# Optimization experiments

Measured on AMD Instinct MI355X. Metric: run time of the kernel, lower is better.

## Reference

```python
import jax, jax.numpy as jnp
import numpy as np

D = 1024       # embedding_dim
H = 4096       # mlp_dim
E = 64         # num_experts
K = 3          # top-k
B, S = 2, 2048
C = 512


def setup_inputs() -> dict:
    key = jax.random.key(0)
    ks = jax.random.split(key, 6)
    s = 0.02
    return {
        "x": jax.random.normal(ks[0], (B, S, D), jnp.float32),
        "gate_w": jax.random.normal(ks[1], (D, E), jnp.float32) * s,
        "gate_b": jnp.zeros((E,), jnp.float32),
        "w1": jax.random.normal(ks[2], (E, D, H), jnp.float32) * s,
        "b1": jnp.zeros((E, H), jnp.float32),
        "w2": jax.random.normal(ks[3], (E, H, D), jnp.float32) * s,
        "b2": jnp.zeros((E, D), jnp.float32),
    }


def reference(x, gate_w, gate_b, w1, b1, w2, b2):
    xf = x.reshape(-1, D)                       # [T, D] flattened tokens
    T = xf.shape[0]
    # --- top-k gating (eval mode: clean logits, no noise) ---
    logits = xf @ gate_w + gate_b               # [T, E]
    top_l, top_i = jax.lax.top_k(logits, K)     # [T, K]
    gates = jax.nn.softmax(top_l, axis=-1)      # softmax over the k selected logits
    # --- token permutation / dispatch (capacity-based, order-preserving) ---
    fe = top_i.reshape(-1)                      # [T*K] expert id per assignment
    fg = gates.reshape(-1)                      # [T*K] gate per assignment
    tok = jnp.repeat(jnp.arange(T), K)          # [T*K] source token id
    oh = jax.nn.one_hot(fe, E, dtype=jnp.int32) # [T*K, E]
    pos = (jnp.cumsum(oh, axis=0) * oh).sum(-1) - 1  # slot within expert buffer
    valid = pos < C                             # capacity mask (C sized so nothing drops in practice)
    # scatter tokens into per-expert buffers; OOB (pos>=C) rows dropped
    buf = jnp.zeros((E, C, D), x.dtype).at[fe, pos].set(xf[tok], mode='drop')
    # --- grouped expert MLP: Linear -> exact GELU -> Linear ---
    h = jax.nn.gelu(jnp.einsum('ecd,edh->ech', buf, w1) + b1[:, None, :], approximate=False)
    y = jnp.einsum('ech,ehd->ecd', h, w2) + b2[:, None, :]  # [E, C, D]
    # --- gather back, gate, scatter-add combine ---
    rows = y[fe, jnp.minimum(pos, C - 1)] * (fg * valid.astype(x.dtype))[:, None]
    out = jnp.zeros_like(xf).at[tok].add(rows)
    return out.reshape(x.shape)
```

## Files before the change

kernel.cpp:

```cpp
#include <hip/hip_runtime.h>

#define TTOK 4096
#define DDIM 1024
#define HDIM 4096
#define NEXP 64
#define CAP  512
#define NASN (TTOK*3)

typedef unsigned short u16;
typedef __attribute__((ext_vector_type(8))) short s16x8;
typedef __attribute__((ext_vector_type(4))) short s16x4;
typedef __attribute__((ext_vector_type(4))) float f32x4;

__device__ __forceinline__ u16 f2bf(float f) {
  union { float f; unsigned u; } v; v.f = f;
  unsigned u = v.u;
  return (u16)((u + 0x7fffu + ((u >> 16) & 1u)) >> 16);
}

__device__ __forceinline__ void gl_lds16(const void* g, void* l) {
  __builtin_amdgcn_global_load_lds(
      (const __attribute__((address_space(1))) void*)g,
      (__attribute__((address_space(3))) void*)l, 16, 0, 0);
}

__global__ __launch_bounds__(256) void zero_out(float4* __restrict__ p, int n4) {
  int i = blockIdx.x * 256 + threadIdx.x;
  int st = gridDim.x * 256;
  for (; i < n4; i += st) p[i] = (float4){0.f, 0.f, 0.f, 0.f};
}

__global__ __launch_bounds__(512) void gate_topk(
    const float* __restrict__ x, const float* __restrict__ gw,
    const float* __restrict__ gb, int* __restrict__ fe, float* __restrict__ fg)
{
  int lane = threadIdx.x & 63;
  int wid  = threadIdx.x >> 6;
  int t = blockIdx.x * 8 + wid;
  const float* xr = x + (size_t)t * DDIM;
  float acc = gb[lane];
  #pragma unroll 4
  for (int d = 0; d < DDIM; d++) acc += xr[d] * gw[d * NEXP + lane];

  float v = acc;
  float bv[3]; int bi[3];
  #pragma unroll
  for (int j = 0; j < 3; j++) {
    float mv = v; int mi = lane;
    #pragma unroll
    for (int off = 32; off; off >>= 1) {
      float ov = __shfl_xor(mv, off);
      int   oi = __shfl_xor(mi, off);
      if (ov > mv || (ov == mv && oi < mi)) { mv = ov; mi = oi; }
    }
    bv[j] = mv; bi[j] = mi;
    if (lane == mi) v = -3.4e38f;
  }
  if (lane == 0) {
    float e1 = expf(bv[1] - bv[0]), e2 = expf(bv[2] - bv[0]);
    float inv = 1.0f / (1.0f + e1 + e2);
    fe[t*3+0] = bi[0]; fe[t*3+1] = bi[1]; fe[t*3+2] = bi[2];
    fg[t*3+0] = inv;   fg[t*3+1] = e1*inv; fg[t*3+2] = e2*inv;
  }
}

__global__ __launch_bounds__(64) void scan_pos(
    const int* __restrict__ fe, int* __restrict__ posA,
    int* __restrict__ s2a, int* __restrict__ cnt)
{
  int e = blockIdx.x, lane = threadIdx.x;
  int base = 0;
  for (int i0 = 0; i0 < NASN; i0 += 64) {
    int i = i0 + lane;
    bool m = (fe[i] == e);
    unsigned long long bal = __ballot(m);
    int below = __popcll(bal & ((1ull << lane) - 1ull));
    if (m) {
      int p = base + below;
      posA[i] = p;
      if (p < CAP) s2a[e * CAP + p] = i;
    }
    base += __popcll(bal);
  }
  if (lane == 0) cnt[e] = base < CAP ? base : CAP;
}

__global__ __launch_bounds__(64) void dispatch(
    const float* __restrict__ x, const int* __restrict__ fe,
    const int* __restrict__ posA, u16* __restrict__ bufA)
{
  int a = blockIdx.x;
  int p = posA[a];
  if (p >= CAP) return;
  int e = fe[a];
  int tok = a / 3;
  int l = threadIdx.x;
  const float4* xr = (const float4*)(x + (size_t)tok * DDIM);
  u16* dst = bufA + ((size_t)e * CAP + p) * DDIM;
  #pragma unroll
  for (int j = 0; j < 4; j++) {
    float4 v = xr[j * 64 + l];
    uint2 u;
    u.x = (unsigned)f2bf(v.x) | ((unsigned)f2bf(v.y) << 16);
    u.y = (unsigned)f2bf(v.z) | ((unsigned)f2bf(v.w) << 16);
    *(uint2*)(dst + (size_t)(j * 64 + l) * 4) = u;
  }
}

template<int KTOT, int NTOT, int EPI>
__global__ __launch_bounds__(256, 2) void moe_gemm(
    const u16* __restrict__ Abuf, const float* __restrict__ W,
    const float* __restrict__ bias, u16* __restrict__ hout,
    float* __restrict__ out, const int* __restrict__ cnt,
    const int* __restrict__ s2a, const float* __restrict__ fg, int g0)
{
  constexpr int NCT = NTOT / 128;
  constexpr int NT  = KTOT / 64;
  int NB = gridDim.x;
  int b = blockIdx.x;
  int L = (b & 7) * (NB >> 3) + (b >> 3);
  int tcol = L % NCT;
  int rt   = (L / NCT) & 1;
  int el   = L / (NCT * 2);
  int e    = g0 + el;
  int cnte = cnt[e];
  int c0   = rt * 256;
  if (c0 >= cnte) return;
  int n0 = tcol * 128;

  int tid = threadIdx.x, l = tid & 63, w = tid >> 6;

  __shared__ char AsB[256 * 128];
  __shared__ char BsB[128 * 136];

  const u16* Arows = Abuf + ((size_t)((EPI == 1 ? e : el)) * CAP + c0) * (size_t)KTOT;
  const float* We = W + (size_t)e * KTOT * NTOT;

  int bn4 = tid & 31, bkb = (tid >> 5) * 8;
  const float* Wt = We + (size_t)bkb * NTOT + n0 + bn4 * 4;
  char* BsW = BsB + (bn4 * 4) * 136 + bkb * 2;

  float4 brB4[8];
  #define LOADB(t) { \
    const float* p_ = Wt + (size_t)(t) * 64 * NTOT; \
    _Pragma("unroll") \
    for (int j_ = 0; j_ < 8; j_++) \
      brB4[j_] = *(const float4*)(p_ + (size_t)j_ * NTOT); \
    }
  #define STOREB() { \
    _Pragma("unroll") \
    for (int c_ = 0; c_ < 4; c_++) { \
      float v0_ = (c_==0?brB4[0].x:c_==1?brB4[0].y:c_==2?brB4[0].z:brB4[0].w); \
      float v1_ = (c_==0?brB4[1].x:c_==1?brB4[1].y:c_==2?brB4[1].z:brB4[1].w); \
      float v2_ = (c_==0?brB4[2].x:c_==1?brB4[2].y:c_==2?brB4[2].z:brB4[2].w); \
      float v3_ = (c_==0?brB4[3].x:c_==1?brB4[3].y:c_==2?brB4[3].z:brB4[3].w); \
      float v4_ = (c_==0?brB4[4].x:c_==1?brB4[4].y:c_==2?brB4[4].z:brB4[4].w); \
      float v5_ = (c_==0?brB4[5].x:c_==1?brB4[5].y:c_==2?brB4[5].z:brB4[5].w); \
      float v6_ = (c_==0?brB4[6].x:c_==1?brB4[6].y:c_==2?brB4[6].z:brB4[6].w); \
      float v7_ = (c_==0?brB4[7].x:c_==1?brB4[7].y:c_==2?brB4[7].z:brB4[7].w); \
      uint2 ua_, ub_; \
      ua_.x = (unsigned)f2bf(v0_) | ((unsigned)f2bf(v1_) << 16); \
      ua_.y = (unsigned)f2bf(v2_) | ((unsigned)f2bf(v3_) << 16); \
      ub_.x = (unsigned)f2bf(v4_) | ((unsigned)f2bf(v5_) << 16); \
      ub_.y = (unsigned)f2bf(v6_) | ((unsigned)f2bf(v7_) << 16); \
      *(uint2*)(BsW + c_ * 136) = ua_; \
      *(uint2*)(BsW + c_ * 136 + 8) = ub_; \
    } }

  f32x4 acc[4][8];
  #pragma unroll
  for (int m = 0; m < 4; m++)
    #pragma unroll
    for (int nn = 0; nn < 8; nn++)
      acc[m][nn] = (f32x4){0.f, 0.f, 0.f, 0.f};

  LOADB(0);

  for (int t = 0; t < NT; ++t) {
    #pragma unroll
    for (int i = 0; i < 8; i++) {
      int r = i * 32 + w * 8 + (l >> 3);
      int cswz = (l & 7) ^ (r & 7);
      const char* gsrc = (const char*)(Arows + (size_t)r * KTOT + (size_t)t * 64) + cswz * 16;
      gl_lds16(gsrc, AsB + (i * 32 + w * 8) * 128);
    }
    STOREB();
    __builtin_amdgcn_sched_barrier(0);
    if (t + 1 < NT) {
      LOADB(t + 1);
      __builtin_amdgcn_sched_barrier(0);
      asm volatile("s_waitcnt vmcnt(8)" ::: "memory");
    } else {
      asm volatile("s_waitcnt vmcnt(0)" ::: "memory");
    }
    asm volatile("s_waitcnt lgkmcnt(0)" ::: "memory");
    __builtin_amdgcn_sched_barrier(0);
    __builtin_amdgcn_s_barrier();
    __builtin_amdgcn_sched_barrier(0);

    #pragma unroll
    for (int k2 = 0; k2 < 2; k2++) {
      int kb = k2 * 32;
      s16x8 af[4], bf8[8];
      #pragma unroll
      for (int m = 0; m < 4; m++) {
        int R = w * 64 + m * 16 + (l & 15);
        int chunk = (kb >> 3) + (l >> 4);
        int sc = chunk ^ (R & 7);
        af[m] = *(const s16x8*)(AsB + R * 128 + sc * 16);
      }
      #pragma unroll
      for (int nn = 0; nn < 8; nn++) {
        int Nn = nn * 16 + (l & 15);
        int kk = kb + (l >> 4) * 8;
        const char* bp = BsB + Nn * 136 + kk * 2;
        union { s16x8 v8; s16x4 v4[2]; } bu;
        bu.v4[0] = *(const s16x4*)bp;
        bu.v4[1] = *(const s16x4*)(bp + 8);
        bf8[nn] = bu.v8;
      }
      #pragma unroll
      for (int m = 0; m < 4; m++)
        #pragma unroll
        for (int nn = 0; nn < 8; nn++)
          acc[m][nn] = __builtin_amdgcn_mfma_f32_16x16x32_bf16(af[m], bf8[nn], acc[m][nn], 0, 0, 0);
    }
    __builtin_amdgcn_s_barrier();
    __builtin_amdgcn_sched_barrier(0);
  }

  int lr = l >> 4, lc = l & 15;
  float bv[8];
  #pragma unroll
  for (int nn = 0; nn < 8; nn++) bv[nn] = bias[(size_t)e * NTOT + n0 + nn * 16 + lc];

  if (EPI == 1) {
    #pragma unroll
    for (int m = 0; m < 4; m++)
      #pragma unroll
      for (int q = 0; q < 4; q++) {
        int rowL = w * 64 + m * 16 + lr * 4 + q;
        if (c0 + rowL < cnte) {
          #pragma unroll
          for (int nn = 0; nn < 8; nn++) {
            float vv = acc[m][nn][q] + bv[nn];
            vv = 0.5f * vv * (1.0f + erff(vv * 0.70710678118f));
            hout[(size_t)(el * CAP + c0 + rowL) * NTOT + (n0 + nn * 16 + lc)] = f2bf(vv);
          }
        }
      }
  } else {
    #pragma unroll
    for (int m = 0; m < 4; m++) {
      int rowbase = w * 64 + m * 16 + lr * 4;
      #pragma unroll
      for (int q = 0; q < 4; q++) {
        int slot = c0 + rowbase + q;
        if (slot < cnte) {
          int aidx = s2a[e * CAP + slot];
          int tok = aidx / 3;
          float gg = fg[aidx];
          #pragma unroll
          for (int nn = 0; nn < 8; nn++) {
            float vv = (acc[m][nn][q] + bv[nn]) * gg;
            atomicAdd(out + (size_t)tok * DDIM + (n0 + nn * 16 + lc), vv);
          }
        }
      }
    }
  }
}

extern "C" void kernel_launch(void* const* d_in, const int* in_sizes, int n_in,
                              void* d_out, int out_size, void* d_ws, size_t ws_size,
                              hipStream_t stream) {
  (void)in_sizes; (void)n_in; (void)ws_size;
  const float* x  = (const float*)d_in[0];
  const float* gw = (const float*)d_in[1];
  const float* gb = (const float*)d_in[2];
  const float* w1 = (const float*)d_in[3];
  const float* b1 = (const float*)d_in[4];
  const float* w2 = (const float*)d_in[5];
  const float* b2 = (const float*)d_in[6];
  float* out = (float*)d_out;

  char* ws = (char*)d_ws;
  int*   fe   = (int*)(ws);
  float* fg   = (float*)(ws + 49152);
  int*   posA = (int*)(ws + 98304);
  int*   s2a  = (int*)(ws + 147456);
  int*   cnt  = (int*)(ws + 278528);
  u16*   bufA = (u16*)(ws + (1 << 20));
  u16*   hbuf = (u16*)(ws + (1 << 20) + 67108864ull);

  zero_out<<<1024, 256, 0, stream>>>((float4*)out, out_size / 4);
  gate_topk<<<TTOK / 8, 512, 0, stream>>>(x, gw, gb, fe, fg);
  scan_pos<<<NEXP, 64, 0, stream>>>(fe, posA, s2a, cnt);
  dispatch<<<NASN, 64, 0, stream>>>(x, fe, posA, bufA);

  moe_gemm<DDIM, HDIM, 1><<<NEXP * 2 * (HDIM / 128), 256, 0, stream>>>(
      bufA, w1, b1, hbuf, nullptr, cnt, nullptr, nullptr, 0);
  moe_gemm<HDIM, DDIM, 2><<<NEXP * 2 * (DDIM / 128), 256, 0, stream>>>(
      hbuf, w2, b2, nullptr, out, cnt, s2a, fg, 0);
}
```

Baseline: 694.4 us.

## Prefetch next A tile during MFMA and swizzle B LDS layout

Each wave now loads only the 64 A rows it consumes. It pulls its A fragments into registers for both k-halves, then issues the global-to-LDS loads for the next A tile before running the MFMAs. This overlaps A-tile latency with compute instead of serializing it at the top of each iteration. The padded 136-byte B stride is replaced by an unpadded 128-byte row with an XOR swizzle, which cuts LDS footprint and aims to avoid bank conflicts. In exchange, more A fragment registers stay live and there are extra lgkmcnt waits.

```diff
diff --git a/kernel.cpp b/kernel.cpp
--- a/kernel.cpp
+++ b/kernel.cpp
@@ -22,6 +22,10 @@
   __builtin_amdgcn_global_load_lds(
       (const __attribute__((address_space(1))) void*)g,
       (__attribute__((address_space(3))) void*)l, 16, 0, 0);
+}
+
+__device__ __forceinline__ int bswz(int row) {
+  return (((row >> 2) ^ ((row & 3) << 2)) & 15) << 3;
 }
 
 __global__ __launch_bounds__(256) void zero_out(float4* __restrict__ p, int n4) {
@@ -131,14 +135,13 @@
   int tid = threadIdx.x, l = tid & 63, w = tid >> 6;
 
   __shared__ char AsB[256 * 128];
-  __shared__ char BsB[128 * 136];
+  __shared__ char BsB[128 * 128];
 
   const u16* Arows = Abuf + ((size_t)((EPI == 1 ? e : el)) * CAP + c0) * (size_t)KTOT;
   const float* We = W + (size_t)e * KTOT * NTOT;
 
   int bn4 = tid & 31, bkb = (tid >> 5) * 8;
   const float* Wt = We + (size_t)bkb * NTOT + n0 + bn4 * 4;
-  char* BsW = BsB + (bn4 * 4) * 136 + bkb * 2;
 
   float4 brB4[8];
   #define LOADB(t) { \
@@ -163,9 +166,24 @@
       ua_.y = (unsigned)f2bf(v2_) | ((unsigned)f2bf(v3_) << 16); \
       ub_.x = (unsigned)f2bf(v4_) | ((unsigned)f2bf(v5_) << 16); \
       ub_.y = (unsigned)f2bf(v6_) | ((unsigned)f2bf(v7_) << 16); \
-      *(uint2*)(BsW + c_ * 136) = ua_; \
-      *(uint2*)(BsW + c_ * 136 + 8) = ub_; \
+      int row_ = bn4 * 4 + c_; \
+      int sw_  = bswz(row_); \
+      char* rb_ = BsB + row_ * 128; \
+      *(uint2*)(rb_ + ((bkb * 2) ^ sw_))     = ua_; \
+      *(uint2*)(rb_ + ((bkb * 2 + 8) ^ sw_)) = ub_; \
     } }
+
+  #define GLDS_A(t) { \
+    _Pragma("unroll") \
+    for (int i_ = 0; i_ < 8; i_++) { \
+      int rb_ = w * 64 + i_ * 8; \
+      int r_  = rb_ + (l >> 3); \
+      int cswz_ = (l & 7) ^ (r_ & 7); \
+      const char* gsrc_ = (const char*)(Arows + (size_t)r_ * KTOT + (size_t)(t) * 64) + cswz_ * 16; \
+      gl_lds16(gsrc_, AsB + rb_ * 128); \
+    } }
+
+  #define SB() __builtin_amdgcn_sched_barrier(0)
 
   f32x4 acc[4][8];
   #pragma unroll
@@ -174,59 +192,66 @@
     for (int nn = 0; nn < 8; nn++)
       acc[m][nn] = (f32x4){0.f, 0.f, 0.f, 0.f};
 
+  GLDS_A(0);
   LOADB(0);
 
   for (int t = 0; t < NT; ++t) {
-    #pragma unroll
-    for (int i = 0; i < 8; i++) {
-      int r = i * 32 + w * 8 + (l >> 3);
-      int cswz = (l & 7) ^ (r & 7);
-      const char* gsrc = (const char*)(Arows + (size_t)r * KTOT + (size_t)t * 64) + cswz * 16;
-      gl_lds16(gsrc, AsB + (i * 32 + w * 8) * 128);
-    }
     STOREB();
-    __builtin_amdgcn_sched_barrier(0);
+    SB();
     if (t + 1 < NT) {
       LOADB(t + 1);
-      __builtin_amdgcn_sched_barrier(0);
+      SB();
       asm volatile("s_waitcnt vmcnt(8)" ::: "memory");
     } else {
       asm volatile("s_waitcnt vmcnt(0)" ::: "memory");
     }
     asm volatile("s_waitcnt lgkmcnt(0)" ::: "memory");
-    __builtin_amdgcn_sched_barrier(0);
+    SB();
     __builtin_amdgcn_s_barrier();
-    __builtin_amdgcn_sched_barrier(0);
-
-    #pragma unroll
-    for (int k2 = 0; k2 < 2; k2++) {
-      int kb = k2 * 32;
-      s16x8 af[4], bf8[8];
+    SB();
+
+    {
+      s16x8 af[4][2];
       #pragma unroll
-      for (int m = 0; m < 4; m++) {
-        int R = w * 64 + m * 16 + (l & 15);
-        int chunk = (kb >> 3) + (l >> 4);
-        int sc = chunk ^ (R & 7);
-        af[m] = *(const s16x8*)(AsB + R * 128 + sc * 16);
+      for (int k2 = 0; k2 < 2; k2++) {
+        #pragma unroll
+        for (int m = 0; m < 4; m++) {
+          int R = w * 64 + m * 16 + (l & 15);
+          int chunk = k2 * 4 + (l >> 4);
+          int sc = chunk ^ (R & 7);
+          af[m][k2] = *(const s16x8*)(AsB + R * 128 + sc * 16);
+        }
       }
+      asm volatile("s_waitcnt lgkmcnt(0)" ::: "memory");
+      SB();
+      if (t + 1 < NT) { GLDS_A(t + 1); }
+      SB();
       #pragma unroll
-      for (int nn = 0; nn < 8; nn++) {
-        int Nn = nn * 16 + (l & 15);
-        int kk = kb + (l >> 4) * 8;
-        const char* bp = BsB + Nn * 136 + kk * 2;
-        union { s16x8 v8; s16x4 v4[2]; } bu;
-        bu.v4[0] = *(const s16x4*)bp;
-        bu.v4[1] = *(const s16x4*)(bp + 8);
-        bf8[nn] = bu.v8;
+      for (int k2 = 0; k2 < 2; k2++) {
+        int kb = k2 * 32;
+        s16x8 bf8[8];
+        #pragma unroll
+        for (int nn = 0; nn < 8; nn++) {
+          int Nn = nn * 16 + (l & 15);
+          int kk = kb + (l >> 4) * 8;
+          int o1 = (kk * 2) ^ bswz(Nn);
+          const char* bp = BsB + Nn * 128;
+          union { s16x8 v8; s16x4 v4[2]; } bu;
+          bu.v4[0] = *(const s16x4*)(bp + o1);
+          bu.v4[1] = *(const s16x4*)(bp + (o1 ^ 8));
+          bf8[nn] = bu.v8;
+        }
+        #pragma unroll
+        for (int m = 0; m < 4; m++)
+          #pragma unroll
+          for (int nn = 0; nn < 8; nn++)
+            acc[m][nn] = __builtin_amdgcn_mfma_f32_16x16x32_bf16(af[m][k2], bf8[nn], acc[m][nn], 0, 0, 0);
       }
-      #pragma unroll
-      for (int m = 0; m < 4; m++)
-        #pragma unroll
-        for (int nn = 0; nn < 8; nn++)
-          acc[m][nn] = __builtin_amdgcn_mfma_f32_16x16x32_bf16(af[m], bf8[nn], acc[m][nn], 0, 0, 0);
-    }
+    }
+    asm volatile("s_waitcnt lgkmcnt(0)" ::: "memory");
+    SB();
     __builtin_amdgcn_s_barrier();
-    __builtin_amdgcn_sched_barrier(0);
+    SB();
   }
 
   int lr = l >> 4, lc = l & 15;
```

Measured after the change: 1.072 ms. +54.4%, slower.

## Replace atomic scatter-add combine with per-expert store plus gather combine kernel

Applied to the files above, without the earlier changes.

The second expert GEMM now writes plain fp32 rows into a per-expert output buffer instead of atomically adding gated rows into the output. A new combine kernel gathers each token's three expert rows, applies the gate weights and writes the output directly, so the zero-fill kernel is no longer needed. This trades global atomic contention for an extra fp32 write and read of the expert output buffer plus one more kernel launch.

```diff
diff --git a/kernel.cpp b/kernel.cpp
--- a/kernel.cpp
+++ b/kernel.cpp
@@ -22,12 +22,6 @@
   __builtin_amdgcn_global_load_lds(
       (const __attribute__((address_space(1))) void*)g,
       (__attribute__((address_space(3))) void*)l, 16, 0, 0);
-}
-
-__global__ __launch_bounds__(256) void zero_out(float4* __restrict__ p, int n4) {
-  int i = blockIdx.x * 256 + threadIdx.x;
-  int st = gridDim.x * 256;
-  for (; i < n4; i += st) p[i] = (float4){0.f, 0.f, 0.f, 0.f};
 }
 
 __global__ __launch_bounds__(512) void gate_topk(
@@ -107,12 +101,32 @@
   }
 }
 
+__global__ __launch_bounds__(256) void combine(
+    const float* __restrict__ y, const int* __restrict__ fe,
+    const float* __restrict__ fg, const int* __restrict__ posA,
+    float* __restrict__ out)
+{
+  int t = blockIdx.x;
+  int d4 = threadIdx.x;
+  float4 s = (float4){0.f, 0.f, 0.f, 0.f};
+  #pragma unroll
+  for (int k = 0; k < 3; k++) {
+    int a = t * 3 + k;
+    int p = posA[a];
+    if (p < CAP) {
+      float g = fg[a];
+      float4 v = *(const float4*)(y + ((size_t)fe[a] * CAP + p) * DDIM + d4 * 4);
+      s.x += g * v.x; s.y += g * v.y; s.z += g * v.z; s.w += g * v.w;
+    }
+  }
+  *(float4*)(out + (size_t)t * DDIM + d4 * 4) = s;
+}
+
 template<int KTOT, int NTOT, int EPI>
 __global__ __launch_bounds__(256, 2) void moe_gemm(
     const u16* __restrict__ Abuf, const float* __restrict__ W,
     const float* __restrict__ bias, u16* __restrict__ hout,
-    float* __restrict__ out, const int* __restrict__ cnt,
-    const int* __restrict__ s2a, const float* __restrict__ fg, int g0)
+    float* __restrict__ yout, const int* __restrict__ cnt, int g0)
 {
   constexpr int NCT = NTOT / 128;
   constexpr int NT  = KTOT / 64;
@@ -257,14 +271,10 @@
       for (int q = 0; q < 4; q++) {
         int slot = c0 + rowbase + q;
         if (slot < cnte) {
-          int aidx = s2a[e * CAP + slot];
-          int tok = aidx / 3;
-          float gg = fg[aidx];
+          float* yr = yout + ((size_t)e * CAP + slot) * DDIM + n0;
           #pragma unroll
-          for (int nn = 0; nn < 8; nn++) {
-            float vv = (acc[m][nn][q] + bv[nn]) * gg;
-            atomicAdd(out + (size_t)tok * DDIM + (n0 + nn * 16 + lc), vv);
-          }
+          for (int nn = 0; nn < 8; nn++)
+            yr[nn * 16 + lc] = acc[m][nn][q] + bv[nn];
         }
       }
     }
@@ -274,7 +284,7 @@
 extern "C" void kernel_launch(void* const* d_in, const int* in_sizes, int n_in,
                               void* d_out, int out_size, void* d_ws, size_t ws_size,
                               hipStream_t stream) {
-  (void)in_sizes; (void)n_in; (void)ws_size;
+  (void)in_sizes; (void)n_in; (void)ws_size; (void)out_size;
   const float* x  = (const float*)d_in[0];
   const float* gw = (const float*)d_in[1];
   const float* gb = (const float*)d_in[2];
@@ -292,14 +302,16 @@
   int*   cnt  = (int*)(ws + 278528);
   u16*   bufA = (u16*)(ws + (1 << 20));
   u16*   hbuf = (u16*)(ws + (1 << 20) + 67108864ull);
-
-  zero_out<<<1024, 256, 0, stream>>>((float4*)out, out_size / 4);
+  float* ybuf = (float*)(ws + (1 << 20) + 67108864ull + 268435456ull);
+
   gate_topk<<<TTOK / 8, 512, 0, stream>>>(x, gw, gb, fe, fg);
   scan_pos<<<NEXP, 64, 0, stream>>>(fe, posA, s2a, cnt);
   dispatch<<<NASN, 64, 0, stream>>>(x, fe, posA, bufA);
 
   moe_gemm<DDIM, HDIM, 1><<<NEXP * 2 * (HDIM / 128), 256, 0, stream>>>(
-      bufA, w1, b1, hbuf, nullptr, cnt, nullptr, nullptr, 0);
+      bufA, w1, b1, hbuf, nullptr, cnt, 0);
   moe_gemm<HDIM, DDIM, 2><<<NEXP * 2 * (DDIM / 128), 256, 0, stream>>>(
-      hbuf, w2, b2, nullptr, out, cnt, s2a, fg, 0);
-}
+      hbuf, w2, b2, nullptr, ybuf, cnt, 0);
+
+  combine<<<TTOK, 256, 0, stream>>>(ybuf, fe, fg, posA, out);
+}
```

Measured after the change: 692.3 us. About the same (-0.3%).
